# Kernel tuning notes

Measured on AMD Instinct MI355X. Metric: run time of the kernel, lower is better.

## Reference

```python
import jax, jax.numpy as jnp
import numpy as np

# dims: batch, encoder frames, encoder dim, pred-net hidden, joint dim, vocab (blank = V)
B, T, ENC, H, J, V = 32, 64, 1024, 320, 320, 1024
BLANK = V
MAXSYM = 2            # max_symbols_per_step
S = T * MAXSYM        # upper bound on loop-labels iterations (<= MAXSYM steps per frame due to force-blank)


def setup_inputs() -> dict:
    key = jax.random.key(0)
    ks = jax.random.split(key, 10)
    s = 0.05
    return {
        "x": jax.random.normal(ks[0], (B, T, ENC), jnp.float32),
        "out_len": jax.random.randint(ks[1], (B,), T // 2, T + 1, dtype=jnp.int32),
        "W_enc": jax.random.normal(ks[2], (ENC, J), jnp.float32) * s,
        "b_enc": jnp.zeros((J,), jnp.float32),
        "Emb": jax.random.normal(ks[3], (V, H), jnp.float32) * s,
        "W_ih": jax.random.normal(ks[4], (H, 4 * H), jnp.float32) * s,
        "W_hh": jax.random.normal(ks[5], (H, 4 * H), jnp.float32) * s,
        "b_lstm": jnp.zeros((4 * H,), jnp.float32),
        "W_pred": jax.random.normal(ks[6], (H, J), jnp.float32) * s,
        "b_pred": jnp.zeros((J,), jnp.float32),
        "W_out": jax.random.normal(ks[7], (J, V + 1), jnp.float32) * s,
        "b_out": jnp.zeros((V + 1,), jnp.float32),
    }


def _lstm_step(emb, h, c, W_ih, W_hh, b):
    g = emb @ W_ih + h @ W_hh + b
    i, f, gg, o = jnp.split(g, 4, axis=-1)
    c2 = jax.nn.sigmoid(f) * c + jax.nn.sigmoid(i) * jnp.tanh(gg)
    h2 = jax.nn.sigmoid(o) * jnp.tanh(c2)
    return h2, c2


def reference(x, out_len, W_enc, b_enc, Emb, W_ih, W_hh, b_lstm, W_pred, b_pred, W_out, b_out):
    # project_encoder once (as in the torch module)
    x_proj = x @ W_enc + b_enc                      # [B, T, J]
    # SOS step: zero embedding, zero LSTM state (decoder.predict(None, None))
    z = jnp.zeros((B, H), x.dtype)
    h0, c0 = _lstm_step(z, z, z, W_ih, W_hh, b_lstm)
    dec0 = h0 @ W_pred + b_pred                     # project_prednet

    def step(carry, _):
        time, symbols, h, c, dec = carry
        enc_t = jnp.take_along_axis(x_proj, time[:, None, None].astype(jnp.int32), axis=1)[:, 0]  # [B, J]
        logits = jax.nn.relu(enc_t + dec) @ W_out + b_out  # joint_after_projection, [B, V+1]
        scores = logits.max(-1)
        labels = jnp.argmax(logits, -1)
        active = time < out_len
        emit = active & (labels != BLANK)
        # prediction-network step for elements that emitted a non-blank label
        emb = Emb[jnp.where(emit, labels, 0)]
        h2, c2 = _lstm_step(emb, h, c, W_ih, W_hh, b_lstm)
        dec2 = h2 @ W_pred + b_pred
        m = emit[:, None]
        h = jnp.where(m, h2, h)
        c = jnp.where(m, c2, c)
        dec = jnp.where(m, dec2, dec)
        sym2 = jnp.where(emit, symbols + 1, jnp.zeros_like(symbols))
        force = emit & (sym2 >= MAXSYM)             # force blank after max_symbols on one frame
        advance = (active & ~emit) | force          # blank (or forced blank) advances time
        time2 = time + advance.astype(time.dtype)
        sym2 = jnp.where(advance, jnp.zeros_like(sym2), sym2)
        out = (jnp.where(emit, labels, BLANK).astype(jnp.int32),
               jnp.where(active, scores, jnp.zeros_like(scores)),
               time.astype(jnp.int32),
               emit)
        return (time2, sym2, h, c, dec), out

    init = (jnp.zeros((B,), jnp.int32), jnp.zeros((B,), jnp.int32), h0, c0, dec0)
    _, (lab, sc, tm, em) = jax.lax.scan(step, init, None, length=S)
    lengths = em.astype(jnp.int32).sum(0)
    # lab/sc/tm: [S, B] alignment-style records (BLANK filler when nothing emitted);
    # lengths: number of emitted (non-blank) labels per utterance -> equals batched_hyps contents.
    return lab, sc, tm, lengths
```

## Files before the change

kernel.cpp:

```cpp
#include <hip/hip_runtime.h>
#include <math.h>

typedef unsigned long long ull;

constexpr int Bn = 32, Tn = 64, Hn = 320, Jn = 320, Vn = 1024, Sn = 128;
constexpr int G4n = 1280, VP1 = 1025, WO4S = 1028;

constexpr int OFF_XP  = 0;
constexpr int OFF_G   = OFF_XP + Bn*Tn*Jn;
constexpr int OFF_WO4 = OFF_G + Vn*G4n;
constexpr int OFF_WH4 = OFF_WO4 + 80*WO4S*4;
constexpr int OFF_WP4 = OFF_WH4 + 80*G4n*4;
constexpr int OFF_CB  = OFF_WP4 + 80*Jn*4;
constexpr int OFF_DEC = OFF_CB + 2*Bn*Hn;
constexpr int OFF_GB  = OFF_DEC + 2*Bn*Jn;
constexpr int OFF_KEY = OFF_GB + 2*Bn*G4n;
constexpr int OFF_REC = OFF_KEY + 2*Bn*40*2;

__device__ __forceinline__ float sigmf(float x) { return 1.0f / (1.0f + expf(-x)); }

__device__ __forceinline__ ull pack_key(float v, int idx) {
    unsigned u = __float_as_uint(v);
    u = (u & 0x80000000u) ? ~u : (u | 0x80000000u);
    return ((ull)u << 32) | (unsigned)(0x7FFFFFFF - idx);
}
__device__ __forceinline__ float key_val(ull k) {
    unsigned u = (unsigned)(k >> 32);
    return __uint_as_float((u & 0x80000000u) ? (u & 0x7FFFFFFFu) : ~u);
}
__device__ __forceinline__ int key_idx(ull k) { return 0x7FFFFFFF - (int)(k & 0xFFFFFFFFu); }

__device__ __forceinline__ void gemm_tile(const float* __restrict__ A,
                                          const float* __restrict__ Bm,
                                          const float* __restrict__ bias,
                                          float* __restrict__ C,
                                          int M, int N, int K, int bx, int by,
                                          float (*As)[65], float (*Bs)[65]) {
    const int tx = threadIdx.x & 15, ty = threadIdx.x >> 4;
    const int n0 = bx * 64, m0 = by * 64;
    float acc[4][4] = {};
    for (int k0 = 0; k0 < K; k0 += 16) {
        for (int i = threadIdx.x; i < 1024; i += 256) {
            int mm = i >> 4, kk = i & 15;
            As[kk][mm] = A[(m0 + mm) * K + k0 + kk];
            int kk2 = i >> 6, nn = i & 63;
            Bs[kk2][nn] = Bm[(k0 + kk2) * N + n0 + nn];
        }
        __syncthreads();
#pragma unroll
        for (int kk = 0; kk < 16; ++kk) {
            float av[4], bv[4];
#pragma unroll
            for (int r = 0; r < 4; ++r) { av[r] = As[kk][ty * 4 + r]; bv[r] = Bs[kk][tx * 4 + r]; }
#pragma unroll
            for (int i2 = 0; i2 < 4; ++i2)
#pragma unroll
                for (int j2 = 0; j2 < 4; ++j2) acc[i2][j2] += av[i2] * bv[j2];
        }
        __syncthreads();
    }
#pragma unroll
    for (int i2 = 0; i2 < 4; ++i2)
#pragma unroll
        for (int j2 = 0; j2 < 4; ++j2)
            C[(m0 + ty * 4 + i2) * N + n0 + tx * 4 + j2] = acc[i2][j2] + bias[n0 + tx * 4 + j2];
}

__global__ __launch_bounds__(256) void preamble(
    const float* __restrict__ x, const float* __restrict__ W_enc,
    const float* __restrict__ b_enc, const float* __restrict__ Emb,
    const float* __restrict__ W_ih, const float* __restrict__ b_lstm,
    const float* __restrict__ W_hh, const float* __restrict__ W_pred,
    const float* __restrict__ W_out,
    float* __restrict__ xp, float* __restrict__ Gm,
    float* __restrict__ Wo4, float* __restrict__ Wh4, float* __restrict__ Wp4) {
    __shared__ float As[16][65];
    __shared__ float Bs[16][65];
    const int blk = blockIdx.x;
    if (blk < 160) {
        gemm_tile(x, W_enc, b_enc, xp, Bn * Tn, Jn, 1024, blk % 5, blk / 5, As, Bs);
    } else if (blk < 480) {
        const int t = blk - 160;
        gemm_tile(Emb, W_ih, b_lstm, Gm, Vn, G4n, Hn, t % 20, t / 20, As, Bs);
    } else if (blk < 560) {
        const int k4 = blk - 480;
        for (int c = threadIdx.x; c < VP1; c += 256) {
            float4 v;
            v.x = W_out[(k4 * 4 + 0) * VP1 + c];
            v.y = W_out[(k4 * 4 + 1) * VP1 + c];
            v.z = W_out[(k4 * 4 + 2) * VP1 + c];
            v.w = W_out[(k4 * 4 + 3) * VP1 + c];
            ((float4*)Wo4)[(size_t)k4 * WO4S + c] = v;
        }
    } else if (blk < 640) {
        const int k4 = blk - 560;
        for (int c = threadIdx.x; c < G4n; c += 256) {
            float4 v;
            v.x = W_hh[(k4 * 4 + 0) * G4n + c];
            v.y = W_hh[(k4 * 4 + 1) * G4n + c];
            v.z = W_hh[(k4 * 4 + 2) * G4n + c];
            v.w = W_hh[(k4 * 4 + 3) * G4n + c];
            ((float4*)Wh4)[(size_t)k4 * G4n + c] = v;
        }
    } else {
        const int k4 = blk - 640;
        for (int c = threadIdx.x; c < Jn; c += 256) {
            float4 v;
            v.x = W_pred[(k4 * 4 + 0) * Jn + c];
            v.y = W_pred[(k4 * 4 + 1) * Jn + c];
            v.z = W_pred[(k4 * 4 + 2) * Jn + c];
            v.w = W_pred[(k4 * 4 + 3) * Jn + c];
            ((float4*)Wp4)[(size_t)k4 * Jn + c] = v;
        }
    }
}

__global__ __launch_bounds__(320, 1) void rnnt_step(
    const float* __restrict__ xp, const float* __restrict__ Gm,
    const float* __restrict__ Wo4, const float* __restrict__ Wh4,
    const float* __restrict__ Wp4,
    const float* __restrict__ b_out, const float* __restrict__ b_lstm,
    const float* __restrict__ b_pred, const int* __restrict__ out_len,
    float* __restrict__ cb, float* __restrict__ db, float* __restrict__ gb,
    ull* __restrict__ keys, int* __restrict__ rec, float* __restrict__ out,
    int L) {
    __shared__ __align__(16) float h_s[Hn];
    __shared__ __align__(16) float dec_s[Jn];
    __shared__ __align__(16) float f_s[Jn];
    __shared__ ull bk_s;

    const int w = blockIdx.x, tid = threadIdx.x;
    const int b = w & 31, m = w >> 5;
    const int ol = out_len[b];
    const float4* Wo4f = (const float4*)Wo4;
    const float4* Wh4f = (const float4*)Wh4;
    const float4* Wp4f = (const float4*)Wp4;
    const float4* h4 = (const float4*)h_s;
    const float4* f4 = (const float4*)f_s;

    int tnew, genN;
    bool doDec;
    if (L == 0) {
        {
            const int r = tid;
            float c0 = sigmf(b_lstm[r]) * tanhf(b_lstm[2 * Hn + r]);
            float h0 = sigmf(b_lstm[3 * Hn + r]) * tanhf(c0);
            h_s[r] = h0;
            int lc = r - m * 40;
            if (lc >= 0 && lc < 40) cb[b * Hn + r] = c0;
        }
        if (m == 0 && tid == 0) {
            int* rn = rec + b * 4;
            rn[0] = 0; rn[1] = 0; rn[2] = 0;
        }
        __syncthreads();
        tnew = 0; genN = 0; doDec = true;
    } else {
        const int* rp = rec + ((L - 1) & 1) * Bn * 4 + b * 4;
        const int told = rp[0], sold = rp[1], len = rp[2];
        const float* gq = gb + (size_t)((len & 1) * Bn + b) * G4n;
        const float* cv = cb + (size_t)((len & 1) * Bn + b) * Hn;
        float g0 = gq[tid], g1 = gq[Hn + tid], g2 = gq[2 * Hn + tid], g3 = gq[3 * Hn + tid];
        float crv = cv[tid];
        asm volatile("" ::: "memory");
        if (tid < 64) {
            ull k = 0;
            if (tid < 33) k = keys[((L - 1) & 1) * Bn * 40 + b * 40 + tid];
#pragma unroll
            for (int d = 1; d < 64; d <<= 1) {
                ull o = __shfl_xor(k, d, 64);
                if (o > k) k = o;
            }
            if (tid == 0) bk_s = k;
        }
        __syncthreads();
        const ull bk = bk_s;
        const int label = key_idx(bk);
        const bool active = told < ol;
        const bool emit = active && (label != Vn);
        int sym2 = emit ? sold + 1 : 0;
        const bool force = emit && (sym2 >= 2);
        const bool advance = (active && !emit) || force;
        tnew = told + (advance ? 1 : 0);
        sym2 = advance ? 0 : sym2;
        const int newlen = len + (emit ? 1 : 0);
        if (m == 0 && tid == 0) {
            out[(L - 1) * Bn + b] = emit ? (float)label : 1024.0f;
            out[Sn * Bn + (L - 1) * Bn + b] = active ? key_val(bk) : 0.0f;
            out[2 * Sn * Bn + (L - 1) * Bn + b] = (float)told;
            int* rn = rec + (L & 1) * Bn * 4 + b * 4;
            rn[0] = tnew; rn[1] = sym2; rn[2] = newlen;
            if (L == Sn) out[3 * Sn * Bn + b] = (float)newlen;
        }
        if (L == Sn) return;
        if (tnew >= ol) return;
        genN = newlen;
        doDec = emit;
        if (emit) {
            const float* gE = Gm + (size_t)label * G4n;
            float xi = g0 + gE[tid];
            float xf = g1 + gE[Hn + tid];
            float xg = g2 + gE[2 * Hn + tid];
            float xo = g3 + gE[3 * Hn + tid];
            float c2 = sigmf(xf) * crv + sigmf(xi) * tanhf(xg);
            float h2 = sigmf(xo) * tanhf(c2);
            h_s[tid] = h2;
            int lc = tid - m * 40;
            if (lc >= 0 && lc < 40)
                cb[(size_t)((newlen & 1) * Bn + b) * Hn + tid] = c2;
        } else {
            dec_s[tid] = db[(size_t)((len & 1) * Bn + b) * Jn + tid];
        }
        __syncthreads();
    }
    if (doDec) {
        float* dn = db + (size_t)((genN & 1) * Bn + b) * Jn;
        {
            const int c = tid;
            float ax = 0.f, ay = 0.f, az = 0.f, aw = 0.f;
#pragma unroll 20
            for (int k4 = 0; k4 < 80; ++k4) {
                float4 wv = Wp4f[(size_t)k4 * Jn + c];
                float4 hv = h4[k4];
                ax += wv.x * hv.x; ay += wv.y * hv.y;
                az += wv.z * hv.z; aw += wv.w * hv.w;
            }
            float d = b_pred[c] + ax + ay + az + aw;
            dec_s[c] = d;
            int lc = c - m * 40;
            if (lc >= 0 && lc < 40) dn[c] = d;
        }
        if (tid < 160) {
            const int c = m * 160 + tid;
            float ax = 0.f, ay = 0.f, az = 0.f, aw = 0.f;
#pragma unroll 20
            for (int k4 = 0; k4 < 80; ++k4) {
                float4 wv = Wh4f[(size_t)k4 * G4n + c];
                float4 hv = h4[k4];
                ax += wv.x * hv.x; ay += wv.y * hv.y;
                az += wv.z * hv.z; aw += wv.w * hv.w;
            }
            gb[(size_t)((genN & 1) * Bn + b) * G4n + c] = ax + ay + az + aw;
        }
    }
    __syncthreads();
    {
        const int tc = tnew < (Tn - 1) ? tnew : (Tn - 1);
        const float* xr = xp + (size_t)(b * Tn + tc) * Jn;
        f_s[tid] = fmaxf(xr[tid] + dec_s[tid], 0.0f);
    }
    __syncthreads();
    if (tid < 256) {
        const int cl = tid >> 1, kh = tid & 1;
        const int c = m * 128 + cl;
        float ax = 0.f, ay = 0.f, az = 0.f, aw = 0.f;
#pragma unroll 10
        for (int k4 = kh * 40; k4 < kh * 40 + 40; ++k4) {
            float4 wv = Wo4f[(size_t)k4 * WO4S + c];
            float4 fv = f4[k4];
            ax += wv.x * fv.x; ay += wv.y * fv.y;
            az += wv.z * fv.z; aw += wv.w * fv.w;
        }
        float part = ax + ay + az + aw;
        part += __shfl_xor(part, 1, 64);
        ull key = pack_key(part + b_out[c], c);
#pragma unroll
        for (int d = 1; d < 64; d <<= 1) {
            ull o = __shfl_xor(key, d, 64);
            if (o > key) key = o;
        }
        if ((tid & 63) == 0)
            keys[(L & 1) * Bn * 40 + b * 40 + m * 4 + (tid >> 6)] = key;
    } else if (m == 7) {
        const int l = tid - 256;
        float4 wv = Wo4f[(size_t)l * WO4S + Vn];
        float4 fv = f4[l];
        float p = wv.x * fv.x + wv.y * fv.y + wv.z * fv.z + wv.w * fv.w;
        if (l < 16) {
            float4 wv2 = Wo4f[(size_t)(64 + l) * WO4S + Vn];
            float4 fv2 = f4[64 + l];
            p += wv2.x * fv2.x + wv2.y * fv2.y + wv2.z * fv2.z + wv2.w * fv2.w;
        }
#pragma unroll
        for (int d = 1; d < 64; d <<= 1) p += __shfl_xor(p, d, 64);
        if (l == 0) keys[(L & 1) * Bn * 40 + b * 40 + 32] = pack_key(p + b_out[Vn], Vn);
    }
}

extern "C" void kernel_launch(void* const* d_in, const int* in_sizes, int n_in,
                              void* d_out, int out_size, void* d_ws, size_t ws_size,
                              hipStream_t stream) {
    (void)in_sizes; (void)n_in; (void)out_size; (void)ws_size;
    const float* x      = (const float*)d_in[0];
    const int*   outlen = (const int*)d_in[1];
    const float* W_enc  = (const float*)d_in[2];
    const float* b_enc  = (const float*)d_in[3];
    const float* Emb    = (const float*)d_in[4];
    const float* W_ih   = (const float*)d_in[5];
    const float* W_hh   = (const float*)d_in[6];
    const float* b_lstm = (const float*)d_in[7];
    const float* W_pred = (const float*)d_in[8];
    const float* b_pred = (const float*)d_in[9];
    const float* W_out  = (const float*)d_in[10];
    const float* b_out  = (const float*)d_in[11];

    float* ws  = (float*)d_ws;
    float* xp  = ws + OFF_XP;
    float* Gm  = ws + OFF_G;
    float* Wo4 = ws + OFF_WO4;
    float* Wh4 = ws + OFF_WH4;
    float* Wp4 = ws + OFF_WP4;
    float* cb  = ws + OFF_CB;
    float* db  = ws + OFF_DEC;
    float* gb  = ws + OFF_GB;
    ull*   keys = (ull*)(ws + OFF_KEY);
    int*   rec  = (int*)(ws + OFF_REC);

    preamble<<<720, 256, 0, stream>>>(x, W_enc, b_enc, Emb, W_ih, b_lstm,
                                      W_hh, W_pred, W_out,
                                      xp, Gm, Wo4, Wh4, Wp4);

    for (int L = 0; L <= Sn; ++L)
        rnnt_step<<<256, 320, 0, stream>>>(xp, Gm, Wo4, Wh4, Wp4,
                                           b_out, b_lstm, b_pred, outlen,
                                           cb, db, gb, keys, rec,
                                           (float*)d_out, L);
}
```

Baseline: 2.036 ms.

## Split joint output GEMM along K across blocks and reduce partial logits next step

The joint projection is now split along the reduction dimension: each of the 8 blocks per batch row computes its 40-wide slice of the pred-net projection and of relu(enc+dec), then writes partial logits for all 1025 vocab entries. The next step sums the 8 partials plus bias and runs the argmax there. This removes each block's redundant full 320-wide pred projection and full f vector, so each block reads only its own slice of W_pred and W_out, at the cost of writing and re-reading 8x1025 partial logits per batch row every step. The shared-memory A tile in the preamble GEMM is also padded to 68 columns.

```diff
diff --git a/kernel.cpp b/kernel.cpp
--- a/kernel.cpp
+++ b/kernel.cpp
@@ -14,8 +14,8 @@
 constexpr int OFF_CB  = OFF_WP4 + 80*Jn*4;
 constexpr int OFF_DEC = OFF_CB + 2*Bn*Hn;
 constexpr int OFF_GB  = OFF_DEC + 2*Bn*Jn;
-constexpr int OFF_KEY = OFF_GB + 2*Bn*G4n;
-constexpr int OFF_REC = OFF_KEY + 2*Bn*40*2;
+constexpr int OFF_PB  = OFF_GB + 2*Bn*G4n;
+constexpr int OFF_REC = OFF_PB + 2*Bn*8*1028;
 
 __device__ __forceinline__ float sigmf(float x) { return 1.0f / (1.0f + expf(-x)); }
 
@@ -35,7 +35,7 @@
                                           const float* __restrict__ bias,
                                           float* __restrict__ C,
                                           int M, int N, int K, int bx, int by,
-                                          float (*As)[65], float (*Bs)[65]) {
+                                          float (*As)[68], float (*Bs)[65]) {
     const int tx = threadIdx.x & 15, ty = threadIdx.x >> 4;
     const int n0 = bx * 64, m0 = by * 64;
     float acc[4][4] = {};
@@ -74,7 +74,7 @@
     const float* __restrict__ W_out,
     float* __restrict__ xp, float* __restrict__ Gm,
     float* __restrict__ Wo4, float* __restrict__ Wh4, float* __restrict__ Wp4) {
-    __shared__ float As[16][65];
+    __shared__ float As[16][68];
     __shared__ float Bs[16][65];
     const int blk = blockIdx.x;
     if (blk < 160) {
@@ -122,12 +122,12 @@
     const float* __restrict__ b_out, const float* __restrict__ b_lstm,
     const float* __restrict__ b_pred, const int* __restrict__ out_len,
     float* __restrict__ cb, float* __restrict__ db, float* __restrict__ gb,
-    ull* __restrict__ keys, int* __restrict__ rec, float* __restrict__ out,
+    float* __restrict__ pb, int* __restrict__ rec, float* __restrict__ out,
     int L) {
     __shared__ __align__(16) float h_s[Hn];
-    __shared__ __align__(16) float dec_s[Jn];
-    __shared__ __align__(16) float f_s[Jn];
-    __shared__ ull bk_s;
+    __shared__ __align__(16) float f_s[48];
+    __shared__ float dec_s[40];
+    __shared__ ull wk_s[5];
 
     const int w = blockIdx.x, tid = threadIdx.x;
     const int b = w & 31, m = w >> 5;
@@ -136,25 +136,21 @@
     const float4* Wh4f = (const float4*)Wh4;
     const float4* Wp4f = (const float4*)Wp4;
     const float4* h4 = (const float4*)h_s;
-    const float4* f4 = (const float4*)f_s;
 
     int tnew, genN;
     bool doDec;
     if (L == 0) {
-        {
-            const int r = tid;
-            float c0 = sigmf(b_lstm[r]) * tanhf(b_lstm[2 * Hn + r]);
-            float h0 = sigmf(b_lstm[3 * Hn + r]) * tanhf(c0);
-            h_s[r] = h0;
-            int lc = r - m * 40;
-            if (lc >= 0 && lc < 40) cb[b * Hn + r] = c0;
-        }
+        float c0 = sigmf(b_lstm[tid]) * tanhf(b_lstm[2 * Hn + tid]);
+        float h0 = sigmf(b_lstm[3 * Hn + tid]) * tanhf(c0);
+        h_s[tid] = h0;
+        int lc = tid - m * 40;
+        if (lc >= 0 && lc < 40) cb[b * Hn + tid] = c0;
         if (m == 0 && tid == 0) {
             int* rn = rec + b * 4;
             rn[0] = 0; rn[1] = 0; rn[2] = 0;
         }
-        __syncthreads();
         tnew = 0; genN = 0; doDec = true;
+        __syncthreads();
     } else {
         const int* rp = rec + ((L - 1) & 1) * Bn * 4 + b * 4;
         const int told = rp[0], sold = rp[1], len = rp[2];
@@ -163,18 +159,25 @@
         float g0 = gq[tid], g1 = gq[Hn + tid], g2 = gq[2 * Hn + tid], g3 = gq[3 * Hn + tid];
         float crv = cv[tid];
         asm volatile("" ::: "memory");
-        if (tid < 64) {
-            ull k = 0;
-            if (tid < 33) k = keys[((L - 1) & 1) * Bn * 40 + b * 40 + tid];
-#pragma unroll
-            for (int d = 1; d < 64; d <<= 1) {
-                ull o = __shfl_xor(k, d, 64);
-                if (o > k) k = o;
-            }
-            if (tid == 0) bk_s = k;
-        }
-        __syncthreads();
-        const ull bk = bk_s;
+        const float* pp = pb + (size_t)(((L - 1) & 1) * Bn + b) * 8 * 1028;
+        ull key = 0;
+        for (int c = tid; c < VP1; c += 320) {
+            float sv = b_out[c];
+#pragma unroll
+            for (int mm = 0; mm < 8; ++mm) sv += pp[mm * 1028 + c];
+            ull k2 = pack_key(sv, c);
+            if (k2 > key) key = k2;
+        }
+#pragma unroll
+        for (int d = 1; d < 64; d <<= 1) {
+            ull o = __shfl_xor(key, d, 64);
+            if (o > key) key = o;
+        }
+        if ((tid & 63) == 0) wk_s[tid >> 6] = key;
+        __syncthreads();
+        ull bk = wk_s[0];
+#pragma unroll
+        for (int i = 1; i < 5; ++i) if (wk_s[i] > bk) bk = wk_s[i];
         const int label = key_idx(bk);
         const bool active = told < ol;
         const bool emit = active && (label != Vn);
@@ -209,27 +212,12 @@
             if (lc >= 0 && lc < 40)
                 cb[(size_t)((newlen & 1) * Bn + b) * Hn + tid] = c2;
         } else {
-            dec_s[tid] = db[(size_t)((len & 1) * Bn + b) * Jn + tid];
+            if (tid < 40)
+                dec_s[tid] = db[(size_t)((len & 1) * Bn + b) * Jn + m * 40 + tid];
         }
         __syncthreads();
     }
     if (doDec) {
-        float* dn = db + (size_t)((genN & 1) * Bn + b) * Jn;
-        {
-            const int c = tid;
-            float ax = 0.f, ay = 0.f, az = 0.f, aw = 0.f;
-#pragma unroll 20
-            for (int k4 = 0; k4 < 80; ++k4) {
-                float4 wv = Wp4f[(size_t)k4 * Jn + c];
-                float4 hv = h4[k4];
-                ax += wv.x * hv.x; ay += wv.y * hv.y;
-                az += wv.z * hv.z; aw += wv.w * hv.w;
-            }
-            float d = b_pred[c] + ax + ay + az + aw;
-            dec_s[c] = d;
-            int lc = c - m * 40;
-            if (lc >= 0 && lc < 40) dn[c] = d;
-        }
         if (tid < 160) {
             const int c = m * 160 + tid;
             float ax = 0.f, ay = 0.f, az = 0.f, aw = 0.f;
@@ -241,49 +229,45 @@
                 az += wv.z * hv.z; aw += wv.w * hv.w;
             }
             gb[(size_t)((genN & 1) * Bn + b) * G4n + c] = ax + ay + az + aw;
-        }
+        } else if (tid < 200) {
+            const int lc = tid - 160;
+            const int c = m * 40 + lc;
+            float ax = 0.f, ay = 0.f, az = 0.f, aw = 0.f;
+#pragma unroll 20
+            for (int k4 = 0; k4 < 80; ++k4) {
+                float4 wv = Wp4f[(size_t)k4 * Jn + c];
+                float4 hv = h4[k4];
+                ax += wv.x * hv.x; ay += wv.y * hv.y;
+                az += wv.z * hv.z; aw += wv.w * hv.w;
+            }
+            float d = b_pred[c] + ax + ay + az + aw;
+            dec_s[lc] = d;
+            db[(size_t)((genN & 1) * Bn + b) * Jn + c] = d;
+        }
+        __syncthreads();
+    }
+    if (tid < 40) {
+        const int tc = tnew < (Tn - 1) ? tnew : (Tn - 1);
+        f_s[tid] = fmaxf(xp[(size_t)(b * Tn + tc) * Jn + m * 40 + tid] + dec_s[tid], 0.0f);
     }
     __syncthreads();
     {
-        const int tc = tnew < (Tn - 1) ? tnew : (Tn - 1);
-        const float* xr = xp + (size_t)(b * Tn + tc) * Jn;
-        f_s[tid] = fmaxf(xr[tid] + dec_s[tid], 0.0f);
-    }
-    __syncthreads();
-    if (tid < 256) {
-        const int cl = tid >> 1, kh = tid & 1;
-        const int c = m * 128 + cl;
-        float ax = 0.f, ay = 0.f, az = 0.f, aw = 0.f;
-#pragma unroll 10
-        for (int k4 = kh * 40; k4 < kh * 40 + 40; ++k4) {
-            float4 wv = Wo4f[(size_t)k4 * WO4S + c];
-            float4 fv = f4[k4];
-            ax += wv.x * fv.x; ay += wv.y * fv.y;
-            az += wv.z * fv.z; aw += wv.w * fv.w;
-        }
-        float part = ax + ay + az + aw;
-        part += __shfl_xor(part, 1, 64);
-        ull key = pack_key(part + b_out[c], c);
-#pragma unroll
-        for (int d = 1; d < 64; d <<= 1) {
-            ull o = __shfl_xor(key, d, 64);
-            if (o > key) key = o;
-        }
-        if ((tid & 63) == 0)
-            keys[(L & 1) * Bn * 40 + b * 40 + m * 4 + (tid >> 6)] = key;
-    } else if (m == 7) {
-        const int l = tid - 256;
-        float4 wv = Wo4f[(size_t)l * WO4S + Vn];
-        float4 fv = f4[l];
-        float p = wv.x * fv.x + wv.y * fv.y + wv.z * fv.z + wv.w * fv.w;
-        if (l < 16) {
-            float4 wv2 = Wo4f[(size_t)(64 + l) * WO4S + Vn];
-            float4 fv2 = f4[64 + l];
-            p += wv2.x * fv2.x + wv2.y * fv2.y + wv2.z * fv2.z + wv2.w * fv2.w;
-        }
-#pragma unroll
-        for (int d = 1; d < 64; d <<= 1) p += __shfl_xor(p, d, 64);
-        if (l == 0) keys[(L & 1) * Bn * 40 + b * 40 + 32] = pack_key(p + b_out[Vn], Vn);
+        const float4* f4 = (const float4*)f_s;
+        float4 fr[10];
+#pragma unroll
+        for (int j = 0; j < 10; ++j) fr[j] = f4[j];
+        float* pw = pb + (size_t)((L & 1) * Bn + b) * 8 * 1028 + m * 1028;
+        for (int c = tid; c < VP1; c += 320) {
+            float ax = 0.f, ay = 0.f, az = 0.f, aw = 0.f;
+#pragma unroll
+            for (int j = 0; j < 10; ++j) {
+                float4 wv = Wo4f[(size_t)(10 * m + j) * WO4S + c];
+                float4 fv = fr[j];
+                ax += wv.x * fv.x; ay += wv.y * fv.y;
+                az += wv.z * fv.z; aw += wv.w * fv.w;
+            }
+            pw[c] = ax + ay + az + aw;
+        }
     }
 }
 
@@ -313,8 +297,8 @@
     float* cb  = ws + OFF_CB;
     float* db  = ws + OFF_DEC;
     float* gb  = ws + OFF_GB;
-    ull*   keys = (ull*)(ws + OFF_KEY);
-    int*   rec  = (int*)(ws + OFF_REC);
+    float* pb  = ws + OFF_PB;
+    int*   rec = (int*)(ws + OFF_REC);
 
     preamble<<<720, 256, 0, stream>>>(x, W_enc, b_enc, Emb, W_ih, b_lstm,
                                       W_hh, W_pred, W_out,
@@ -323,6 +307,6 @@
     for (int L = 0; L <= Sn; ++L)
         rnnt_step<<<256, 320, 0, stream>>>(xp, Gm, Wo4, Wh4, Wp4,
                                            b_out, b_lstm, b_pred, outlen,
-                                           cb, db, gb, keys, rec,
+                                           cb, db, gb, pb, rec,
                                            (float*)d_out, L);
 }
```

New measurement: 1.939 ms. -4.8%, faster.
